# Kernel tuning notes

Measured on AMD Instinct MI355X. Metric: run time of the kernel, lower is better.

## Reference

```python
import jax, jax.numpy as jnp
import numpy as np

JITTER = 1e-6
ND = 20       # num_draws
STEPS = 10    # num_steps
G = 100       # num_gammas: PG truncation terms
NUM_CLASSES = 2


def _rbf(X, outputscale, lengthscale):
    x2 = jnp.sum(X * X, axis=-1)
    d2 = jnp.maximum(x2[:, None] + x2[None, :] - 2.0 * (X @ X.T), 0.0)
    return outputscale * jnp.exp(-0.5 * d2 / (lengthscale * lengthscale))


def _chol(K):
    return jnp.linalg.cholesky(K + JITTER * jnp.eye(K.shape[-1], dtype=K.dtype))


def _pg_draw(key, c):
    # PG(1, c) via truncated infinite gamma convolution (G terms):
    # omega = (1/(2 pi^2)) * sum_k Exp(1) / ((k-1/2)^2 + c^2/(4 pi^2))
    ks = jnp.arange(1, G + 1, dtype=c.dtype)
    denom = (ks - 0.5) ** 2 + (c[..., None] ** 2) / (4.0 * jnp.pi ** 2)
    e = jax.random.exponential(key, c.shape + (G,), dtype=c.dtype)
    return jnp.sum(e / denom, axis=-1) / (2.0 * jnp.pi ** 2)


def reference(X, Y, outputscale, lengthscale):
    N = X.shape[0]
    os_ = outputscale[0]
    ls = lengthscale[0]
    K = _rbf(X, os_, ls)                          # [N,N]
    Kinv = jnp.linalg.inv(K + JITTER * jnp.eye(N, dtype=X.dtype))
    L = _chol(K)
    mu = jnp.zeros((N,), X.dtype)                 # zero mean GP
    Kinv_mu = Kinv @ mu
    y_oh = 1.0 - jax.nn.one_hot(Y, NUM_CLASSES, dtype=X.dtype)
    kappa = y_oh[:, 0] - 0.5                      # binary => 1 stick, N_sb = 1

    key = jax.random.key(42)
    k_init, k_om0, k_loop = jax.random.split(key, 3)

    # initial Gibbs state: f ~ N(mu, K) per draw
    eps0 = jax.random.normal(k_init, (ND, N), X.dtype)
    f = mu[None, :] + jnp.einsum('ij,dj->di', L, eps0)
    omega = jax.lax.stop_gradient(_pg_draw(k_om0, jax.lax.stop_gradient(f)))

    def body(state, kk):
        omega_c, f_c = state
        k1, k2 = jax.random.split(kk)
        A = Kinv[None] + jax.vmap(jnp.diag)(omega_c)         # [ND,N,N]
        sigma = jnp.linalg.inv(A)
        mu_t = jnp.einsum('dij,j->di', sigma, kappa + Kinv_mu)
        Lt = _chol(sigma)
        eps = jax.random.normal(k1, (ND, N), X.dtype)
        f_new = mu_t + jnp.einsum('dij,dj->di', Lt, eps)
        omega_new = jax.lax.stop_gradient(_pg_draw(k2, jax.lax.stop_gradient(f_new)))
        return (omega_new, f_new), None

    (omega, f), _ = jax.lax.scan(body, (omega, f), jax.random.split(k_loop, STEPS))

    # marginal log likelihood given omega (PG draws are constants)
    om = jnp.clip(omega, 1e-16)                  # [ND,N]
    Sigma_z = K[None] + jax.vmap(jnp.diag)(1.0 / om)
    Lz = _chol(Sigma_z)
    z = kappa[None, :] / om
    diff = z - mu[None, :]
    sol = jax.scipy.linalg.solve_triangular(Lz, diff[..., None], lower=True)[..., 0]
    quad = jnp.sum(sol * sol, axis=-1)
    logdet = jnp.sum(jnp.log(jnp.diagonal(Lz, axis1=-2, axis2=-1)), axis=-1)
    log2pi = float(np.log(2.0 * np.pi))
    logp = -0.5 * quad - logdet - 0.5 * N * log2pi
    mll = (logp + 0.5 * N * log2pi
           - 0.5 * jnp.sum(jnp.log(om), axis=-1)
           + 0.5 * jnp.sum(kappa[None, :] ** 2 / om, axis=-1)
           - N * float(np.log(2.0)))
    nmll = -jnp.mean(mll)
    return nmll / N


def setup_inputs() -> dict:
    key = jax.random.key(0)
    kx, ky, ko, kl = jax.random.split(key, 4)
    X = jax.random.normal(kx, (1024, 64), jnp.float32)
    Y = jax.random.randint(ky, (1024,), 0, 2)
    outputscale = jax.random.uniform(ko, (1,), jnp.float32) + 0.5
    # rescale lengthscale to ~sqrt(d) so exp(-d2/2ls^2) doesn't underflow
    lengthscale = (jax.random.uniform(kl, (1,), jnp.float32) + 0.5) * 8.0
    return {"X": X, "Y": Y, "outputscale": outputscale, "lengthscale": lengthscale}
```

## Files before the change

### kernel.cpp

```cpp
#include <hip/hip_runtime.h>
#include <stdint.h>

#define NPTS 1024
#define NDRAWS 20
#define NSTEPS 10
#define NG 100
#define PARTITIONABLE 1

#define TRI(i) (((i) * ((i) + 1)) / 2)
#define NTRI 136
#define AST ((size_t)NTRI * 4096)

typedef unsigned int u32;

__host__ __device__ static inline void tf2x32(u32 k0, u32 k1, u32 x0, u32 x1, u32* o0, u32* o1){
  u32 ks2 = k0 ^ k1 ^ 0x1BD11BDAu;
  x0 += k0; x1 += k1;
#define TFR(r) { x0 += x1; x1 = (x1 << r) | (x1 >> (32 - r)); x1 ^= x0; }
  TFR(13) TFR(15) TFR(26) TFR(6)
  x0 += k1; x1 += ks2 + 1u;
  TFR(17) TFR(29) TFR(16) TFR(24)
  x0 += ks2; x1 += k0 + 2u;
  TFR(13) TFR(15) TFR(26) TFR(6)
  x0 += k0; x1 += k1 + 3u;
  TFR(17) TFR(29) TFR(16) TFR(24)
  x0 += k1; x1 += ks2 + 4u;
  TFR(13) TFR(15) TFR(26) TFR(6)
  x0 += ks2; x1 += k0 + 5u;
#undef TFR
  *o0 = x0; *o1 = x1;
}

__device__ static inline u32 rand32(u32 ka, u32 kb, u32 i, u32 total){
  u32 a, b;
#if PARTITIONABLE
  (void)total;
  tf2x32(ka, kb, 0u, i, &a, &b);
  return a ^ b;
#else
  u32 h = total >> 1;
  if (i < h){ tf2x32(ka, kb, i, i + h, &a, &b); return a; }
  else      { tf2x32(ka, kb, i - h, i, &a, &b); return b; }
#endif
}

__device__ static inline float u01f(u32 bits){
  return __uint_as_float(0x3F800000u | (bits >> 9)) - 1.0f;
}

__device__ static inline float erfinv32(float x){
  float w = -log1pf(-x * x);
  float p;
  if (w < 5.0f){
    w -= 2.5f;
// ... 291 lines not shown
#pragma unroll
      for (int b = 0; b < 4; ++b) ac2[a][b] += av[a] * bv[b];
  }
#pragma unroll
  for (int a = 0; a < 4; ++a)
#pragma unroll
    for (int b = 0; b < 4; ++b)
      Td[(size_t)(I * 64 + ty * 4 + a) * NPTS + J * 64 + tx * 4 + b] = -ac2[a][b];
}

__global__ __launch_bounds__(256) void k_syrk_kinv_flip(const double* Td, float* Kinvp){
  int a0, b0; tri_decode(blockIdx.x, a0, b0);
  int ti = b0, tj = a0;
  int kmin = tj;
  __shared__ double Ta[64][65];
  __shared__ double Tb[64][65];
  int tid = threadIdx.x, tx = tid & 15, ty = tid >> 4;
  double acc[4][4];
#pragma unroll
  for (int a = 0; a < 4; ++a)
#pragma unroll
    for (int b = 0; b < 4; ++b) acc[a][b] = 0.0;
  for (int K = kmin; K < 16; ++K){
    __syncthreads();
    for (int idx = tid; idx < 4096; idx += 256){
      int r = idx >> 6, c = idx & 63;
      Ta[r][c] = Td[(size_t)(K * 64 + r) * NPTS + ti * 64 + c];
      Tb[r][c] = Td[(size_t)(K * 64 + r) * NPTS + tj * 64 + c];
    }
    __syncthreads();
    for (int k = 0; k < 64; ++k){
      double av[4], bv[4];
#pragma unroll
      for (int a = 0; a < 4; ++a) av[a] = Ta[k][ty * 4 + a];
#pragma unroll
      for (int b = 0; b < 4; ++b) bv[b] = Tb[k][tx * 4 + b];
#pragma unroll
      for (int a = 0; a < 4; ++a)
#pragma unroll
        for (int b = 0; b < 4; ++b) acc[a][b] += av[a] * bv[b];
    }
  }
  int tileR = 15 - ti, tileC = 15 - tj;
  float* out = Kinvp + (size_t)(TRI(tileR) + tileC) * 4096;
#pragma unroll
  for (int a = 0; a < 4; ++a)
#pragma unroll
    for (int b = 0; b < 4; ++b){
      int rin = 63 - (ty * 4 + a), cin = 63 - (tx * 4 + b);
      out[rin * 64 + cin] = (float)acc[a][b];
    }
}

__global__ __launch_bounds__(256) void k_buildA(const float* Kinvp, const float* omega, float* Ab,
                                                int c0, int clip){
  int d = c0 + blockIdx.y;
  float* A = Ab + (size_t)blockIdx.y * AST;
  int idx4 = blockIdx.x * 256 + threadIdx.x;
  float4 v = ((const float4*)Kinvp)[idx4];
  int tile = idx4 >> 10;
  int ti, tj; tri_decode(tile, ti, tj);
  if (ti == tj){
    int e = (idx4 & 1023) * 4;
    int r = e >> 6, c = e & 63;
    if (c <= r && r < c + 4){
      float om = omega[(size_t)d * NPTS + (NPTS - 1 - (ti * 64 + r))];
      if (clip) om = fmaxf(om, 1e-16f);
      ((float*)&v)[r - c] += om;
    }
  }
  ((float4*)A)[idx4] = v;
}

__global__ __launch_bounds__(256) void k_diag0(float* Ab, float* Dinv){
  float* M = Ab + (size_t)blockIdx.x * AST;
  float* DI = Dinv + (size_t)blockIdx.x * 16 * 4096;
  __shared__ float t[64][65];
  __shared__ float Xs[64][65];
  __shared__ float diagL[64];
  int tid = threadIdx.x;
  for (int idx = tid; idx < 1024; idx += 256){
    float4 v = ((const float4*)M)[idx];
    int e = idx * 4, r = e >> 6, c = e & 63;
    t[r][c] = v.x; t[r][c + 1] = v.y; t[r][c + 2] = v.z; t[r][c + 3] = v.w;
  }
  __syncthreads();
  chol_inv_64t<float, 65>(&t[0][0], &Xs[0][0], &diagL[0], tid);
  for (int idx = tid; idx < 1024; idx += 256){
    int e = idx * 4, r = e >> 6, c = e & 63;
    float4 v, w;
    v.x = (c     <= r) ? t[r][c]     : 0.f;
    v.y = (c + 1 <= r) ? t[r][c + 1] : 0.f;
    v.z = (c + 2 <= r) ? t[r][c + 2] : 0.f;
    v.w = (c + 3 <= r) ? t[r][c + 3] : 0.f;
    w.x = Xs[r][c]; w.y = Xs[r][c + 1]; w.z = Xs[r][c + 2]; w.w = Xs[r][c + 3];
    ((float4*)M)[idx] = v;
    ((float4*)DI)[idx] = w;
  }
}

__global__ __launch_bounds__(256) void k_panel(float* Ab, const float* Dinv, int p){
  float* M = Ab + (size_t)blockIdx.y * AST;
  const float* DI = Dinv + ((size_t)blockIdx.y * 16 + p) * 4096;
  int rt = p + 1 + blockIdx.x;
  float* R = M + (size_t)(TRI(rt) + p) * 4096;
  __shared__ __align__(16) float Rst[64 * 68];
  __shared__ __align__(16) float Dst[64 * 68];
  int tid = threadIdx.x;
  for (int idx = tid; idx < 1024; idx += 256){
    float4 v = ((const float4*)R)[idx];
    float4 w = ((const float4*)DI)[idx];
    int e = idx * 4, r = e >> 6, c = e & 63;
    Rst[(c + 0) * 68 + r] = v.x; Rst[(c + 1) * 68 + r] = v.y;
    Rst[(c + 2) * 68 + r] = v.z; Rst[(c + 3) * 68 + r] = v.w;
    Dst[(c + 0) * 68 + r] = w.x; Dst[(c + 1) * 68 + r] = w.y;
    Dst[(c + 2) * 68 + r] = w.z; Dst[(c + 3) * 68 + r] = w.w;
  }
  __syncthreads();
  int tx = tid & 15, ty = tid >> 4;
  float acc[4][4];
#pragma unroll
  for (int a = 0; a < 4; ++a)
#pragma unroll
    for (int b = 0; b < 4; ++b) acc[a][b] = 0.f;
  for (int k = 0; k < 64; ++k){
    float4 av4 = *(const float4*)&Rst[k * 68 + ty * 4];
    float4 bv4 = *(const float4*)&Dst[k * 68 + tx * 4];
    float av[4] = {av4.x, av4.y, av4.z, av4.w};
    float bv[4] = {bv4.x, bv4.y, bv4.z, bv4.w};
#pragma unroll
    for (int a = 0; a < 4; ++a)
#pragma unroll
      for (int b = 0; b < 4; ++b) acc[a][b] += av[a] * bv[b];
  }
#pragma unroll
  for (int a = 0; a < 4; ++a){
    float4 v;
    v.x = acc[a][0]; v.y = acc[a][1]; v.z = acc[a][2]; v.w = acc[a][3];
    *((float4*)&R[(size_t)(ty * 4 + a) * 64 + tx * 4]) = v;
  }
}

__global__ __launch_bounds__(256) void k_update_diag(float* Ab, float* Dinv, int p){
  float* M = Ab + (size_t)blockIdx.y * AST;
  __shared__ __align__(16) float Pat[64 * 68];
  __shared__ __align__(16) float Pbt[64 * 68];
  __shared__ float diagL[64];
  int t0, t1; tri_decode(blockIdx.x, t0, t1);
  int bi = p + 1 + t0, bj = p + 1 + t1;
  const float* La = M + (size_t)(TRI(bi) + p) * 4096;
  const float* Lb = M + (size_t)(TRI(bj) + p) * 4096;
  float* Atile = M + (size_t)(TRI(bi) + bj) * 4096;
  int tid = threadIdx.x;
  for (int idx = tid; idx < 1024; idx += 256){
    float4 v = ((const float4*)La)[idx];
    float4 w = ((const float4*)Lb)[idx];
    int e = idx * 4, r = e >> 6, c = e & 63;
    Pat[(c + 0) * 68 + r] = v.x; Pat[(c + 1) * 68 + r] = v.y;
    Pat[(c + 2) * 68 + r] = v.z; Pat[(c + 3) * 68 + r] = v.w;
    Pbt[(c + 0) * 68 + r] = w.x; Pbt[(c + 1) * 68 + r] = w.y;
    Pbt[(c + 2) * 68 + r] = w.z; Pbt[(c + 3) * 68 + r] = w.w;
  }
  __syncthreads();
  int tx = tid & 15, ty = tid >> 4;
  float acc[4][4];
#pragma unroll
  for (int a = 0; a < 4; ++a)
#pragma unroll
    for (int b = 0; b < 4; ++b) acc[a][b] = 0.f;
  for (int k = 0; k < 64; ++k){
    float4 av4 = *(const float4*)&Pat[k * 68 + ty * 4];
    float4 bv4 = *(const float4*)&Pbt[k * 68 + tx * 4];
    float av[4] = {av4.x, av4.y, av4.z, av4.w};
    float bv[4] = {bv4.x, bv4.y, bv4.z, bv4.w};
#pragma unroll
    for (int a = 0; a < 4; ++a)
#pragma unroll
      for (int b = 0; b < 4; ++b) acc[a][b] += av[a] * bv[b];
  }
  if (blockIdx.x == 0){
    __syncthreads();
    for (int idx = tid; idx < 1024; idx += 256){
      float4 v = ((const float4*)Atile)[idx];
      int e = idx * 4, r = e >> 6, c = e & 63;
      Pat[r * 68 + c] = v.x; Pat[r * 68 + c + 1] = v.y;
      Pat[r * 68 + c + 2] = v.z; Pat[r * 68 + c + 3] = v.w;
    }
    __syncthreads();
#pragma unroll
    for (int a = 0; a < 4; ++a)
#pragma unroll
      for (int b = 0; b < 4; ++b)
        Pat[(ty * 4 + a) * 68 + tx * 4 + b] -= acc[a][b];
    __syncthreads();
    chol_inv_64t<float, 68>(Pat, Pbt, &diagL[0], tid);
    float* DI = Dinv + ((size_t)blockIdx.y * 16 + (p + 1)) * 4096;
    for (int idx = tid; idx < 1024; idx += 256){
      int e = idx * 4, r = e >> 6, c = e & 63;
      float4 v, w;
      v.x = (c     <= r) ? Pat[r * 68 + c]     : 0.f;
      v.y = (c + 1 <= r) ? Pat[r * 68 + c + 1] : 0.f;
      v.z = (c + 2 <= r) ? Pat[r * 68 + c + 2] : 0.f;
      v.w = (c + 3 <= r) ? Pat[r * 68 + c + 3] : 0.f;
      w.x = Pbt[r * 68 + c]; w.y = Pbt[r * 68 + c + 1];
      w.z = Pbt[r * 68 + c + 2]; w.w = Pbt[r * 68 + c + 3];
      ((float4*)Atile)[idx] = v;
      ((float4*)DI)[idx] = w;
    }
  } else {
#pragma unroll
    for (int a = 0; a < 4; ++a){
      float4 v = *((const float4*)&Atile[(size_t)(ty * 4 + a) * 64 + tx * 4]);
      v.x -= acc[a][0]; v.y -= acc[a][1]; v.z -= acc[a][2]; v.w -= acc[a][3];
      *((float4*)&Atile[(size_t)(ty * 4 + a) * 64 + tx * 4]) = v;
    }
  }
}

static void run_chol_f(float* A, float* Dinv, int batch, hipStream_t s){
  k_diag0<<<dim3(batch), 256, 0, s>>>(A, Dinv);
  for (int p = 0; p < 15; ++p){
    int nrb = 15 - p;
    k_panel<<<dim3(nrb, batch), 256, 0, s>>>(A, Dinv, p);
    k_update_diag<<<dim3(nrb * (nrb + 1) / 2, batch), 256, 0, s>>>(A, Dinv, p);
  }
}

__global__ __launch_bounds__(256) void k_step_solve(const float* Ab, const float* DinvF,
                                                    const float* kappaf, const float* eps,
                                                    float* fbuf, int c0){
  int d0 = blockIdx.x, d = c0 + d0;
  const float* L = Ab + (size_t)d0 * AST;
  const float* DI = DinvF + (size_t)d0 * 16 * 4096;
  __shared__ float z1[NPTS], z2[NPTS];
  __shared__ float buf[2][64 * 65];
  __shared__ float p1[4][64], p2[4][64];
  int tid = threadIdx.x;
  float4 rg[4];
  auto loadDI = [&](int p){
#pragma unroll
    for (int j = 0; j < 4; ++j)
      rg[j] = *(const float4*)&DI[p * 4096 + j * 1024 + tid * 4];
  };
  auto loadL = [&](int row, int col){
    const float* T = L + (size_t)(TRI(row) + col) * 4096;
#pragma unroll
    for (int j = 0; j < 4; ++j)
      rg[j] = *(const float4*)&T[j * 1024 + tid * 4];
  };
  auto store = [&](int cur){
#pragma unroll
    for (int j = 0; j < 4; ++j){
      int e = j * 1024 + tid * 4; int r = e >> 6, c = e & 63;
      float* b = &buf[cur][r * 65 + c];
      b[0] = rg[j].x; b[1] = rg[j].y; b[2] = rg[j].z; b[3] = rg[j].w;
    }
  };
  for (int i = tid; i < NPTS; i += 256){
    z1[i] = kappaf[i];
    z2[NPTS - 1 - i] = eps[(size_t)d * NPTS + i];
  }
  loadDI(0);
  int cur = 0;
  for (int p = 0; p < 16; ++p){
    for (int rb = p; rb < 16; ++rb){
      store(cur);
      int np = p, nrb = rb + 1;
      if (nrb >= 16){ np = p + 1; nrb = np; }
      if (np < 16){ if (nrb == np) loadDI(np); else loadL(nrb, np); }
      __syncthreads();
      int rr = tid & 63, q = tid >> 6;
      float s = 0.f;
#pragma unroll
      for (int cc = 0; cc < 16; ++cc)
        s += buf[cur][rr * 65 + q * 16 + cc] * z1[p * 64 + q * 16 + cc];
      p1[q][rr] = s;
      __syncthreads();
      if (tid < 64){
        float v = p1[0][tid] + p1[1][tid] + p1[2][tid] + p1[3][tid];
        if (rb == p) z1[p * 64 + tid] = v;
        else z1[rb * 64 + tid] -= v;
      }
      __syncthreads();
      cur ^= 1;
    }
  }
  loadDI(15);
  for (int p = 15; p >= 0; --p){
    for (int cb = p; cb >= 0; --cb){
      store(cur);
      int np = p, ncb = cb - 1;
      if (ncb < 0){ np = p - 1; ncb = np; }
      if (np >= 0){ if (ncb == np) loadDI(np); else loadL(np, ncb); }
      __syncthreads();
      int cc = tid & 63, q = tid >> 6;
      float s1 = 0.f, s2 = 0.f;
#pragma unroll
      for (int rr = 0; rr < 16; ++rr){
        float t = buf[cur][(q * 16 + rr) * 65 + cc];
        s1 += t * z1[p * 64 + q * 16 + rr];
        s2 += t * z2[p * 64 + q * 16 + rr];
      }
      p1[q][cc] = s1; p2[q][cc] = s2;
      __syncthreads();
      if (tid < 64){
        float v1 = p1[0][tid] + p1[1][tid] + p1[2][tid] + p1[3][tid];
        float v2 = p2[0][tid] + p2[1][tid] + p2[2][tid] + p2[3][tid];
        if (cb == p){ z1[p * 64 + tid] = v1; z2[p * 64 + tid] = v2; }
        else { z1[cb * 64 + tid] -= v1; z2[cb * 64 + tid] -= v2; }
      }
      __syncthreads();
      cur ^= 1;
    }
  }
  for (int i = tid; i < NPTS; i += 256)
    fbuf[(size_t)d * NPTS + i] = z1[NPTS - 1 - i] + z2[NPTS - 1 - i];
}

__global__ __launch_bounds__(256) void k_final3(const float* Ab, const float* DinvF,
                                                const float* kappaf, const float* ldetK,
                                                float* mll, int c0){
  int d0 = blockIdx.x, d = c0 + d0;
  const float* L = Ab + (size_t)d0 * AST;
  const float* DI = DinvF + (size_t)d0 * 16 * 4096;
  __shared__ float z[NPTS];
  __shared__ float buf[2][64 * 65];
  __shared__ float part[4][64];
  __shared__ float redq[4];
  int tid = threadIdx.x;
  float4 rg[4];
  auto loadDI = [&](int p){
#pragma unroll
    for (int j = 0; j < 4; ++j)
      rg[j] = *(const float4*)&DI[p * 4096 + j * 1024 + tid * 4];
  };
  auto loadL = [&](int rbrow, int pcol){
    const float* T = L + (size_t)(TRI(rbrow) + pcol) * 4096;
#pragma unroll
    for (int j = 0; j < 4; ++j)
      rg[j] = *(const float4*)&T[j * 1024 + tid * 4];
  };
  auto store = [&](int cur){
#pragma unroll
    for (int j = 0; j < 4; ++j){
      int e = j * 1024 + tid * 4; int r = e >> 6, c = e & 63;
      float* b = &buf[cur][r * 65 + c];
      b[0] = rg[j].x; b[1] = rg[j].y; b[2] = rg[j].z; b[3] = rg[j].w;
    }
  };
  for (int i = tid; i < NPTS; i += 256) z[i] = kappaf[i];
  loadDI(0);
  int cur = 0;
  float ldacc = 0.f;
  for (int p = 0; p < 16; ++p){
    for (int rb = p; rb < 16; ++rb){
      store(cur);
      int np = p, nrb = rb + 1;
      if (nrb >= 16){ np = p + 1; nrb = np; }
      if (np < 16){ if (nrb == np) loadDI(np); else loadL(nrb, np); }
      __syncthreads();
      if (rb == p && tid < 64) ldacc += logf(buf[cur][tid * 65 + tid]);
      int rr = tid & 63, q = tid >> 6;
      float s = 0.f;
#pragma unroll
      for (int cc = 0; cc < 16; ++cc)
        s += buf[cur][rr * 65 + q * 16 + cc] * z[p * 64 + q * 16 + cc];
      part[q][rr] = s;
      __syncthreads();
      if (tid < 64){
        float v = part[0][tid] + part[1][tid] + part[2][tid] + part[3][tid];
        if (rb == p) z[p * 64 + tid] = v;
        else z[rb * 64 + tid] -= v;
      }
      __syncthreads();
      cur ^= 1;
    }
  }
  float q2 = 0.f;
  for (int i = tid; i < NPTS; i += 256) q2 += z[i] * z[i];
  int wid = tid >> 6, lane = tid & 63;
  for (int o = 32; o; o >>= 1) q2 += __shfl_down(q2, o);
  if (lane == 0) redq[wid] = q2;
  __syncthreads();
  if (tid < 64){
    float ldv = ldacc;
    for (int o = 32; o; o >>= 1) ldv += __shfl_down(ldv, o);
    if (tid == 0){
      float q2t = redq[0] + redq[1] + redq[2] + redq[3];
      mll[d] = 0.5f * q2t + ldv - 0.5f * ldetK[0] - 709.7827128933839f;
    }
  }
}

__global__ __launch_bounds__(256) void k_gen_eps(u32 ka, u32 kb, float* eps){
  int i = blockIdx.x * 256 + threadIdx.x;
  if (i >= NDRAWS * NPTS) return;
  u32 bits = rand32(ka, kb, (u32)i, (u32)(NDRAWS * NPTS));
  eps[i] = normal_from_bits(bits);
}

__global__ __launch_bounds__(256) void k_init_f2(const float* Lf, const float* eps, float* f){
  int d = blockIdx.y, rb = blockIdx.x;
  __shared__ float tile[64][65];
  __shared__ float ev[64];
  __shared__ float part[4][64];
  int tid = threadIdx.x;
  int r = tid & 63, q = tid >> 6;
  float acc = 0.f;
  for (int kt = 0; kt <= rb; ++kt){
    __syncthreads();
#pragma unroll
    for (int j = 0; j < 4; ++j){
      int e = j * 1024 + tid * 4; int rr = e >> 6, cc = e & 63;
      float4 v = *(const float4*)&Lf[(size_t)(rb * 64 + rr) * NPTS + kt * 64 + cc];
      tile[rr][cc] = v.x; tile[rr][cc + 1] = v.y; tile[rr][cc + 2] = v.z; tile[rr][cc + 3] = v.w;
    }
    if (tid < 64) ev[tid] = eps[(size_t)d * NPTS + kt * 64 + tid];
    __syncthreads();
    int cmax = (kt == rb) ? (r + 1) : 64;
    for (int cc = q * 16; cc < q * 16 + 16; ++cc){
      if (cc < cmax) acc += tile[r][cc] * ev[cc];
    }
  }
  part[q][r] = acc;
  __syncthreads();
  if (tid < 64){
    float s = part[0][tid] + part[1][tid] + part[2][tid] + part[3][tid];
    f[(size_t)d * NPTS + rb * 64 + tid] = s;
  }
}

__global__ __launch_bounds__(256) void k_pg(u32 ka, u32 kb, const float* f, float* omega){
  int idx = blockIdx.x * 256 + threadIdx.x;
  if (idx >= NDRAWS * NPTS) return;
  float c = f[idx];
  float c2w = (c * c) / 39.47841760435743f;
  float sum = 0.f;
  u32 base = (u32)idx * NG;
  for (int g = 0; g < NG; ++g){
    u32 bits = rand32(ka, kb, base + (u32)g, (u32)(NDRAWS * NPTS * NG));
    float u = u01f(bits);
    float e = -log1pf(-u);
    float kk = (float)g + 0.5f;
// ... 25 lines not shown
}

extern "C" void kernel_launch(void* const* d_in, const int* in_sizes, int n_in,
                              void* d_out, int out_size, void* d_ws, size_t ws_size,
                              hipStream_t stream){
  const float* X  = (const float*)d_in[0];
  const int*   Y  = (const int*)d_in[1];
  const float* osp = (const float*)d_in[2];
  const float* lsp = (const float*)d_in[3];
  float* out = (float*)d_out;

  const size_t NN = (size_t)NPTS * NPTS;
  char* p = (char*)d_ws;
  float* Kinvp  = (float*)p;  p += AST * 4;
  float* omega  = (float*)p;  p += (size_t)NDRAWS * NPTS * 4;
  float* fbuf   = (float*)p;  p += (size_t)NDRAWS * NPTS * 4;
  float* epsb   = (float*)p;  p += (size_t)NDRAWS * NPTS * 4;
  float* kappaf = (float*)p;  p += NPTS * 4;
  float* x2     = (float*)p;  p += NPTS * 4;
  float* mll    = (float*)p;  p += 128;
  float* ldetK  = (float*)p;  p += 128;
  uintptr_t ip = (uintptr_t)p; ip = (ip + 255) & ~(uintptr_t)255;
  char* cb = (char*)ip;

  double* Ld    = (double*)cb;
  double* Td    = (double*)(cb + NN * 8);
  double* DinvD = (double*)(cb + NN * 16);
  float*  Lf    = (float*)(cb + NN * 16 + (size_t)16 * 4096 * 8);
  double* Gslc  = (double*)(cb + NN * 16 + (size_t)16 * 4096 * 8 + NN * 4);

  size_t rem = ws_size - (size_t)(cb - (char*)d_ws);
  const size_t PER_DRAW = AST * 4 + (size_t)16 * 4096 * 4;
  int CH = (int)(rem / PER_DRAW);
  if (CH > NDRAWS) CH = NDRAWS;
  if (CH < 1) CH = 1;
  float* bufA  = (float*)cb;
  float* dinvF = (float*)(cb + (size_t)CH * AST * 4);

  u32 r3A[3], r3B[3];
  host_split(0u, 42u, 3, r3A, r3B);
  u32 kiA = r3A[0], kiB = r3B[0];
  u32 koA = r3A[1], koB = r3B[1];
  u32 klA = r3A[2], klB = r3B[2];
  u32 kkA[NSTEPS], kkB[NSTEPS];
  host_split(klA, klB, NSTEPS, kkA, kkB);
  u32 k1A[NSTEPS], k1B[NSTEPS], k2A[NSTEPS], k2B[NSTEPS];
  for (int t = 0; t < NSTEPS; ++t){
    u32 sA[2], sB[2];
    host_split(kkA[t], kkB[t], 2, sA, sB);
    k1A[t] = sA[0]; k1B[t] = sB[0];
    k2A[t] = sA[1]; k2B[t] = sB[1];
  }

  k_prep<<<dim3(4), 256, 0, stream>>>(X, Y, x2, kappaf);
  k_computeK<<<dim3(64, 64), dim3(16, 16), 0, stream>>>(X, x2, osp, lsp, Ld);
  run_chol_d(Ld, DinvD, stream);
  k_castL<<<dim3(4096), 256, 0, stream>>>(Ld, Lf);
  k_logdetK<<<dim3(1), 256, 0, stream>>>(Ld, ldetK);
  k_trinv_copy_diag<<<dim3(16), 256, 0, stream>>>(DinvD, Td);
  for (int lev = 1; lev < 16; ++lev){
    k_trinv_part<<<dim3(16 - lev, lev), 256, 0, stream>>>(Ld, Td, Gslc, lev);
    k_trinv_fin<<<dim3(16 - lev), 256, 0, stream>>>(Td, Gslc, lev);
  }
  k_syrk_kinv_flip<<<dim3(NTRI), 256, 0, stream>>>(Td, Kinvp);

  k_gen_eps<<<dim3(80), 256, 0, stream>>>(kiA, kiB, epsb);
  k_init_f2<<<dim3(16, NDRAWS), 256, 0, stream>>>(Lf, epsb, fbuf);
  k_pg<<<dim3(80), 256, 0, stream>>>(koA, koB, fbuf, omega);

  for (int t = 0; t < NSTEPS; ++t){
    k_gen_eps<<<dim3(80), 256, 0, stream>>>(k1A[t], k1B[t], epsb);
    for (int c0 = 0; c0 < NDRAWS; c0 += CH){
      int nb = NDRAWS - c0 < CH ? NDRAWS - c0 : CH;
      k_buildA<<<dim3(544, nb), 256, 0, stream>>>(Kinvp, omega, bufA, c0, 0);
      run_chol_f(bufA, dinvF, nb, stream);
      k_step_solve<<<dim3(nb), 256, 0, stream>>>(bufA, dinvF, kappaf, epsb, fbuf, c0);
    }
    k_pg<<<dim3(80), 256, 0, stream>>>(k2A[t], k2B[t], fbuf, omega);
  }

  for (int c0 = 0; c0 < NDRAWS; c0 += CH){
    int nb = NDRAWS - c0 < CH ? NDRAWS - c0 : CH;
    k_buildA<<<dim3(544, nb), 256, 0, stream>>>(Kinvp, omega, bufA, c0, 1);
    run_chol_f(bufA, dinvF, nb, stream);
    k_final3<<<dim3(nb), 256, 0, stream>>>(bufA, dinvF, kappaf, ldetK, mll, c0);
  }
  k_out<<<dim3(1), 64, 0, stream>>>(mll, out);
}
```

Baseline: 23.16 ms.

## Fuse per-step Gibbs kernels into one persistent cooperative kernel with grid syncs

The eps generation, A assembly, blocked Cholesky (diag/panel/update phases), solve and PG draw for each chunk are merged into a single cooperative kernel. Grid-wide syncs separate the phases instead of dozens of separate kernel launches. This is meant to remove launch overhead and tail gaps across the roughly 30 launches per chunk per step. In exchange, grid size is capped at a few blocks per CU, and each grid.sync has its own cost. Phases with little work, like diag0 with nb blocks, leave most blocks idle.

```diff
diff --git a/kernel.cpp b/kernel.cpp
--- a/kernel.cpp
+++ b/kernel.cpp
@@ -1,5 +1,8 @@
 #include <hip/hip_runtime.h>
+#include <hip/hip_cooperative_groups.h>
 #include <stdint.h>
+
+namespace cg = cooperative_groups;
 
 #define NPTS 1024
 #define NDRAWS 20
@@ -397,343 +400,422 @@
     }
 }
 
-__global__ __launch_bounds__(256) void k_buildA(const float* Kinvp, const float* omega, float* Ab,
-                                                int c0, int clip){
-  int d = c0 + blockIdx.y;
-  float* A = Ab + (size_t)blockIdx.y * AST;
-  int idx4 = blockIdx.x * 256 + threadIdx.x;
-  float4 v = ((const float4*)Kinvp)[idx4];
-  int tile = idx4 >> 10;
-  int ti, tj; tri_decode(tile, ti, tj);
-  if (ti == tj){
-    int e = (idx4 & 1023) * 4;
-    int r = e >> 6, c = e & 63;
-    if (c <= r && r < c + 4){
-      float om = omega[(size_t)d * NPTS + (NPTS - 1 - (ti * 64 + r))];
-      if (clip) om = fmaxf(om, 1e-16f);
-      ((float*)&v)[r - c] += om;
-    }
-  }
-  ((float4*)A)[idx4] = v;
-}
-
-__global__ __launch_bounds__(256) void k_diag0(float* Ab, float* Dinv){
-  float* M = Ab + (size_t)blockIdx.x * AST;
-  float* DI = Dinv + (size_t)blockIdx.x * 16 * 4096;
-  __shared__ float t[64][65];
-  __shared__ float Xs[64][65];
-  __shared__ float diagL[64];
-  int tid = threadIdx.x;
-  for (int idx = tid; idx < 1024; idx += 256){
-    float4 v = ((const float4*)M)[idx];
-    int e = idx * 4, r = e >> 6, c = e & 63;
-    t[r][c] = v.x; t[r][c + 1] = v.y; t[r][c + 2] = v.z; t[r][c + 3] = v.w;
-  }
-  __syncthreads();
-  chol_inv_64t<float, 65>(&t[0][0], &Xs[0][0], &diagL[0], tid);
-  for (int idx = tid; idx < 1024; idx += 256){
-    int e = idx * 4, r = e >> 6, c = e & 63;
-    float4 v, w;
-    v.x = (c     <= r) ? t[r][c]     : 0.f;
-    v.y = (c + 1 <= r) ? t[r][c + 1] : 0.f;
-    v.z = (c + 2 <= r) ? t[r][c + 2] : 0.f;
-    v.w = (c + 3 <= r) ? t[r][c + 3] : 0.f;
-    w.x = Xs[r][c]; w.y = Xs[r][c + 1]; w.z = Xs[r][c + 2]; w.w = Xs[r][c + 3];
-    ((float4*)M)[idx] = v;
-    ((float4*)DI)[idx] = w;
-  }
-}
-
-__global__ __launch_bounds__(256) void k_panel(float* Ab, const float* Dinv, int p){
-  float* M = Ab + (size_t)blockIdx.y * AST;
-  const float* DI = Dinv + ((size_t)blockIdx.y * 16 + p) * 4096;
-  int rt = p + 1 + blockIdx.x;
-  float* R = M + (size_t)(TRI(rt) + p) * 4096;
-  __shared__ __align__(16) float Rst[64 * 68];
-  __shared__ __align__(16) float Dst[64 * 68];
-  int tid = threadIdx.x;
-  for (int idx = tid; idx < 1024; idx += 256){
-    float4 v = ((const float4*)R)[idx];
-    float4 w = ((const float4*)DI)[idx];
-    int e = idx * 4, r = e >> 6, c = e & 63;
-    Rst[(c + 0) * 68 + r] = v.x; Rst[(c + 1) * 68 + r] = v.y;
-    Rst[(c + 2) * 68 + r] = v.z; Rst[(c + 3) * 68 + r] = v.w;
-    Dst[(c + 0) * 68 + r] = w.x; Dst[(c + 1) * 68 + r] = w.y;
-    Dst[(c + 2) * 68 + r] = w.z; Dst[(c + 3) * 68 + r] = w.w;
-  }
-  __syncthreads();
-  int tx = tid & 15, ty = tid >> 4;
-  float acc[4][4];
-#pragma unroll
-  for (int a = 0; a < 4; ++a)
-#pragma unroll
-    for (int b = 0; b < 4; ++b) acc[a][b] = 0.f;
-  for (int k = 0; k < 64; ++k){
-    float4 av4 = *(const float4*)&Rst[k * 68 + ty * 4];
-    float4 bv4 = *(const float4*)&Dst[k * 68 + tx * 4];
-    float av[4] = {av4.x, av4.y, av4.z, av4.w};
-    float bv[4] = {bv4.x, bv4.y, bv4.z, bv4.w};
-#pragma unroll
-    for (int a = 0; a < 4; ++a)
-#pragma unroll
-      for (int b = 0; b < 4; ++b) acc[a][b] += av[a] * bv[b];
-  }
-#pragma unroll
-  for (int a = 0; a < 4; ++a){
-    float4 v;
-    v.x = acc[a][0]; v.y = acc[a][1]; v.z = acc[a][2]; v.w = acc[a][3];
-    *((float4*)&R[(size_t)(ty * 4 + a) * 64 + tx * 4]) = v;
-  }
-}
-
-__global__ __launch_bounds__(256) void k_update_diag(float* Ab, float* Dinv, int p){
-  float* M = Ab + (size_t)blockIdx.y * AST;
-  __shared__ __align__(16) float Pat[64 * 68];
-  __shared__ __align__(16) float Pbt[64 * 68];
-  __shared__ float diagL[64];
-  int t0, t1; tri_decode(blockIdx.x, t0, t1);
-  int bi = p + 1 + t0, bj = p + 1 + t1;
-  const float* La = M + (size_t)(TRI(bi) + p) * 4096;
-  const float* Lb = M + (size_t)(TRI(bj) + p) * 4096;
-  float* Atile = M + (size_t)(TRI(bi) + bj) * 4096;
-  int tid = threadIdx.x;
-  for (int idx = tid; idx < 1024; idx += 256){
-    float4 v = ((const float4*)La)[idx];
-    float4 w = ((const float4*)Lb)[idx];
-    int e = idx * 4, r = e >> 6, c = e & 63;
-    Pat[(c + 0) * 68 + r] = v.x; Pat[(c + 1) * 68 + r] = v.y;
-    Pat[(c + 2) * 68 + r] = v.z; Pat[(c + 3) * 68 + r] = v.w;
-    Pbt[(c + 0) * 68 + r] = w.x; Pbt[(c + 1) * 68 + r] = w.y;
-    Pbt[(c + 2) * 68 + r] = w.z; Pbt[(c + 3) * 68 + r] = w.w;
-  }
-  __syncthreads();
-  int tx = tid & 15, ty = tid >> 4;
-  float acc[4][4];
-#pragma unroll
-  for (int a = 0; a < 4; ++a)
-#pragma unroll
-    for (int b = 0; b < 4; ++b) acc[a][b] = 0.f;
-  for (int k = 0; k < 64; ++k){
-    float4 av4 = *(const float4*)&Pat[k * 68 + ty * 4];
-    float4 bv4 = *(const float4*)&Pbt[k * 68 + tx * 4];
-    float av[4] = {av4.x, av4.y, av4.z, av4.w};
-    float bv[4] = {bv4.x, bv4.y, bv4.z, bv4.w};
-#pragma unroll
-    for (int a = 0; a < 4; ++a)
-#pragma unroll
-      for (int b = 0; b < 4; ++b) acc[a][b] += av[a] * bv[b];
-  }
-  if (blockIdx.x == 0){
-    __syncthreads();
+
+__device__ inline void ph_geneps(u32 ka, u32 kb, float* eps, int c0, int nb, int tid){
+  int total = nb * NPTS;
+  for (int b0 = blockIdx.x * 256; b0 < total; b0 += gridDim.x * 256){
+    int i = b0 + tid;
+    if (i < total){
+      int g = c0 * NPTS + i;
+      u32 bits = rand32(ka, kb, (u32)g, (u32)(NDRAWS * NPTS));
+      eps[g] = normal_from_bits(bits);
+    }
+  }
+}
+
+__device__ inline void ph_pg(u32 ka, u32 kb, const float* f, float* omega, int c0, int nb, int tid){
+  int total = nb * NPTS;
+  for (int b0 = blockIdx.x * 256; b0 < total; b0 += gridDim.x * 256){
+    int i = b0 + tid;
+    if (i < total){
+      int gidx = c0 * NPTS + i;
+      float c = f[gidx];
+      float c2w = (c * c) / 39.47841760435743f;
+      float sum = 0.f;
+      u32 base = (u32)gidx * NG;
+      for (int g = 0; g < NG; ++g){
+        u32 bits = rand32(ka, kb, base + (u32)g, (u32)(NDRAWS * NPTS * NG));
+        float u = u01f(bits);
+        float e = -log1pf(-u);
+        float kk = (float)g + 0.5f;
+        sum += e / (kk * kk + c2w);
+      }
+      omega[gidx] = sum / 19.739208802178716f;
+    }
+  }
+}
+
+__device__ inline void ph_buildA(const float* Kinvp, const float* omega, float* Ab,
+                                 int c0, int nb, int clip, int tid){
+  for (int task = blockIdx.x; task < 544 * nb; task += gridDim.x){
+    int dd = task / 544, blk = task - dd * 544;
+    int d = c0 + dd;
+    float* A = Ab + (size_t)dd * AST;
+    int idx4 = blk * 256 + tid;
+    float4 v = ((const float4*)Kinvp)[idx4];
+    int tile = idx4 >> 10;
+    int ti, tj; tri_decode(tile, ti, tj);
+    if (ti == tj){
+      int e = (idx4 & 1023) * 4;
+      int r = e >> 6, c = e & 63;
+      if (c <= r && r < c + 4){
+        float om = omega[(size_t)d * NPTS + (NPTS - 1 - (ti * 64 + r))];
+        if (clip) om = fmaxf(om, 1e-16f);
+        ((float*)&v)[r - c] += om;
+      }
+    }
+    ((float4*)A)[idx4] = v;
+  }
+}
+
+__device__ inline void ph_diag0(float* Ab, float* Dinv, int nb, int tid,
+                                float* shT, float* shX, float* dgl){
+  for (int task = blockIdx.x; task < nb; task += gridDim.x){
+    float* M = Ab + (size_t)task * AST;
+    float* DI = Dinv + (size_t)task * 16 * 4096;
     for (int idx = tid; idx < 1024; idx += 256){
-      float4 v = ((const float4*)Atile)[idx];
+      float4 v = ((const float4*)M)[idx];
       int e = idx * 4, r = e >> 6, c = e & 63;
-      Pat[r * 68 + c] = v.x; Pat[r * 68 + c + 1] = v.y;
-      Pat[r * 68 + c + 2] = v.z; Pat[r * 68 + c + 3] = v.w;
-    }
-    __syncthreads();
-#pragma unroll
-    for (int a = 0; a < 4; ++a)
-#pragma unroll
-      for (int b = 0; b < 4; ++b)
-        Pat[(ty * 4 + a) * 68 + tx * 4 + b] -= acc[a][b];
-    __syncthreads();
-    chol_inv_64t<float, 68>(Pat, Pbt, &diagL[0], tid);
-    float* DI = Dinv + ((size_t)blockIdx.y * 16 + (p + 1)) * 4096;
+      shT[r * 68 + c] = v.x; shT[r * 68 + c + 1] = v.y;
+      shT[r * 68 + c + 2] = v.z; shT[r * 68 + c + 3] = v.w;
+    }
+    __syncthreads();
+    chol_inv_64t<float, 68>(shT, shX, dgl, tid);
     for (int idx = tid; idx < 1024; idx += 256){
       int e = idx * 4, r = e >> 6, c = e & 63;
       float4 v, w;
-      v.x = (c     <= r) ? Pat[r * 68 + c]     : 0.f;
-      v.y = (c + 1 <= r) ? Pat[r * 68 + c + 1] : 0.f;
-      v.z = (c + 2 <= r) ? Pat[r * 68 + c + 2] : 0.f;
-      v.w = (c + 3 <= r) ? Pat[r * 68 + c + 3] : 0.f;
-      w.x = Pbt[r * 68 + c]; w.y = Pbt[r * 68 + c + 1];
-      w.z = Pbt[r * 68 + c + 2]; w.w = Pbt[r * 68 + c + 3];
-      ((float4*)Atile)[idx] = v;
+      v.x = (c     <= r) ? shT[r * 68 + c]     : 0.f;
+      v.y = (c + 1 <= r) ? shT[r * 68 + c + 1] : 0.f;
+      v.z = (c + 2 <= r) ? shT[r * 68 + c + 2] : 0.f;
+      v.w = (c + 3 <= r) ? shT[r * 68 + c + 3] : 0.f;
+      w.x = shX[r * 68 + c]; w.y = shX[r * 68 + c + 1];
+      w.z = shX[r * 68 + c + 2]; w.w = shX[r * 68 + c + 3];
+      ((float4*)M)[idx] = v;
       ((float4*)DI)[idx] = w;
     }
+    __syncthreads();
+  }
+}
+
+__device__ inline void ph_panel(float* Ab, const float* Dinv, int p, int nb, int tid,
+                                float* Rst, float* Dst){
+  int nrb = 15 - p;
+  int tx = tid & 15, ty = tid >> 4;
+  for (int task = blockIdx.x; task < nrb * nb; task += gridDim.x){
+    int dd = task / nrb, rto = task - dd * nrb;
+    float* M = Ab + (size_t)dd * AST;
+    const float* DI = Dinv + ((size_t)dd * 16 + p) * 4096;
+    int rt = p + 1 + rto;
+    float* R = M + (size_t)(TRI(rt) + p) * 4096;
+    for (int idx = tid; idx < 1024; idx += 256){
+      float4 v = ((const float4*)R)[idx];
+      float4 w = ((const float4*)DI)[idx];
+      int e = idx * 4, r = e >> 6, c = e & 63;
+      Rst[(c + 0) * 68 + r] = v.x; Rst[(c + 1) * 68 + r] = v.y;
+      Rst[(c + 2) * 68 + r] = v.z; Rst[(c + 3) * 68 + r] = v.w;
+      Dst[(c + 0) * 68 + r] = w.x; Dst[(c + 1) * 68 + r] = w.y;
+      Dst[(c + 2) * 68 + r] = w.z; Dst[(c + 3) * 68 + r] = w.w;
+    }
+    __syncthreads();
+    float acc[4][4];
+#pragma unroll
+    for (int a = 0; a < 4; ++a)
+#pragma unroll
+      for (int b = 0; b < 4; ++b) acc[a][b] = 0.f;
+    for (int k = 0; k < 64; ++k){
+      float4 av4 = *(const float4*)&Rst[k * 68 + ty * 4];
+      float4 bv4 = *(const float4*)&Dst[k * 68 + tx * 4];
+      float av[4] = {av4.x, av4.y, av4.z, av4.w};
+      float bv[4] = {bv4.x, bv4.y, bv4.z, bv4.w};
+#pragma unroll
+      for (int a = 0; a < 4; ++a)
+#pragma unroll
+        for (int b = 0; b < 4; ++b) acc[a][b] += av[a] * bv[b];
+    }
+#pragma unroll
+    for (int a = 0; a < 4; ++a){
+      float4 v;
+      v.x = acc[a][0]; v.y = acc[a][1]; v.z = acc[a][2]; v.w = acc[a][3];
+      *((float4*)&R[(size_t)(ty * 4 + a) * 64 + tx * 4]) = v;
+    }
+    __syncthreads();
+  }
+}
+
+__device__ inline void ph_update(float* Ab, float* Dinv, int p, int nb, int tid,
+                                 float* Pat, float* Pbt, float* dgl){
+  int nrb = 15 - p;
+  int ntri = nrb * (nrb + 1) / 2;
+  int tx = tid & 15, ty = tid >> 4;
+  for (int task = blockIdx.x; task < ntri * nb; task += gridDim.x){
+    int dd = task / ntri, tri = task - dd * ntri;
+    float* M = Ab + (size_t)dd * AST;
+    int t0, t1; tri_decode(tri, t0, t1);
+    int bi = p + 1 + t0, bj = p + 1 + t1;
+    const float* La = M + (size_t)(TRI(bi) + p) * 4096;
+    const float* Lb = M + (size_t)(TRI(bj) + p) * 4096;
+    float* Atile = M + (size_t)(TRI(bi) + bj) * 4096;
+    for (int idx = tid; idx < 1024; idx += 256){
+      float4 v = ((const float4*)La)[idx];
+      float4 w = ((const float4*)Lb)[idx];
+      int e = idx * 4, r = e >> 6, c = e & 63;
+      Pat[(c + 0) * 68 + r] = v.x; Pat[(c + 1) * 68 + r] = v.y;
+      Pat[(c + 2) * 68 + r] = v.z; Pat[(c + 3) * 68 + r] = v.w;
+      Pbt[(c + 0) * 68 + r] = w.x; Pbt[(c + 1) * 68 + r] = w.y;
+      Pbt[(c + 2) * 68 + r] = w.z; Pbt[(c + 3) * 68 + r] = w.w;
+    }
+    __syncthreads();
+    float acc[4][4];
+#pragma unroll
+    for (int a = 0; a < 4; ++a)
+#pragma unroll
+      for (int b = 0; b < 4; ++b) acc[a][b] = 0.f;
+    for (int k = 0; k < 64; ++k){
+      float4 av4 = *(const float4*)&Pat[k * 68 + ty * 4];
+      float4 bv4 = *(const float4*)&Pbt[k * 68 + tx * 4];
+      float av[4] = {av4.x, av4.y, av4.z, av4.w};
+      float bv[4] = {bv4.x, bv4.y, bv4.z, bv4.w};
+#pragma unroll
+      for (int a = 0; a < 4; ++a)
+#pragma unroll
+        for (int b = 0; b < 4; ++b) acc[a][b] += av[a] * bv[b];
+    }
+    if (tri == 0){
+      __syncthreads();
+      for (int idx = tid; idx < 1024; idx += 256){
+        float4 v = ((const float4*)Atile)[idx];
+        int e = idx * 4, r = e >> 6, c = e & 63;
+        Pat[r * 68 + c] = v.x; Pat[r * 68 + c + 1] = v.y;
+        Pat[r * 68 + c + 2] = v.z; Pat[r * 68 + c + 3] = v.w;
+      }
+      __syncthreads();
+#pragma unroll
+      for (int a = 0; a < 4; ++a)
+#pragma unroll
+        for (int b = 0; b < 4; ++b)
+          Pat[(ty * 4 + a) * 68 + tx * 4 + b] -= acc[a][b];
+      __syncthreads();
+      chol_inv_64t<float, 68>(Pat, Pbt, dgl, tid);
+      float* DI = Dinv + ((size_t)dd * 16 + (p + 1)) * 4096;
+      for (int idx = tid; idx < 1024; idx += 256){
+        int e = idx * 4, r = e >> 6, c = e & 63;
+        float4 v, w;
+        v.x = (c     <= r) ? Pat[r * 68 + c]     : 0.f;
+        v.y = (c + 1 <= r) ? Pat[r * 68 + c + 1] : 0.f;
+        v.z = (c + 2 <= r) ? Pat[r * 68 + c + 2] : 0.f;
+        v.w = (c + 3 <= r) ? Pat[r * 68 + c + 3] : 0.f;
+        w.x = Pbt[r * 68 + c]; w.y = Pbt[r * 68 + c + 1];
+        w.z = Pbt[r * 68 + c + 2]; w.w = Pbt[r * 68 + c + 3];
+        ((float4*)Atile)[idx] = v;
+        ((float4*)DI)[idx] = w;
+      }
+      __syncthreads();
+    } else {
+#pragma unroll
+      for (int a = 0; a < 4; ++a){
+        float4 v = *((const float4*)&Atile[(size_t)(ty * 4 + a) * 64 + tx * 4]);
+        v.x -= acc[a][0]; v.y -= acc[a][1]; v.z -= acc[a][2]; v.w -= acc[a][3];
+        *((float4*)&Atile[(size_t)(ty * 4 + a) * 64 + tx * 4]) = v;
+      }
+      __syncthreads();
+    }
+  }
+}
+
+__device__ inline void ph_solve(const float* Ab, const float* DinvF, const float* kappaf,
+                                const float* eps, float* fbuf, int c0, int nb, int tid,
+                                float* smem){
+  float* z1  = smem;
+  float* z2  = smem + 1024;
+  float* bufp = smem + 2048;
+  float* pr1 = smem + 10368;
+  float* pr2 = smem + 10624;
+  for (int task = blockIdx.x; task < nb; task += gridDim.x){
+    int d0 = task, d = c0 + task;
+    const float* L = Ab + (size_t)d0 * AST;
+    const float* DI = DinvF + (size_t)d0 * 16 * 4096;
+    float4 rg[4];
+    auto loadDI = [&](int p){
+#pragma unroll
+      for (int j = 0; j < 4; ++j)
+        rg[j] = *(const float4*)&DI[p * 4096 + j * 1024 + tid * 4];
+    };
+    auto loadL = [&](int row, int col){
+      const float* T = L + (size_t)(TRI(row) + col) * 4096;
+#pragma unroll
+      for (int j = 0; j < 4; ++j)
+        rg[j] = *(const float4*)&T[j * 1024 + tid * 4];
+    };
+    auto store = [&](int cur){
+#pragma unroll
+      for (int j = 0; j < 4; ++j){
+        int e = j * 1024 + tid * 4; int r = e >> 6, c = e & 63;
+        float* b = &bufp[cur * 4160 + r * 65 + c];
+        b[0] = rg[j].x; b[1] = rg[j].y; b[2] = rg[j].z; b[3] = rg[j].w;
+      }
+    };
+    for (int i = tid; i < NPTS; i += 256){
+      z1[i] = kappaf[i];
+      z2[NPTS - 1 - i] = eps[(size_t)d * NPTS + i];
+    }
+    loadDI(0);
+    int cur = 0;
+    for (int p = 0; p < 16; ++p){
+      for (int rb = p; rb < 16; ++rb){
+        store(cur);
+        int np = p, nr2 = rb + 1;
+        if (nr2 >= 16){ np = p + 1; nr2 = np; }
+        if (np < 16){ if (nr2 == np) loadDI(np); else loadL(nr2, np); }
+        __syncthreads();
+        int rr = tid & 63, q = tid >> 6;
+        float s = 0.f;
+#pragma unroll
+        for (int cc = 0; cc < 16; ++cc)
+          s += bufp[cur * 4160 + rr * 65 + q * 16 + cc] * z1[p * 64 + q * 16 + cc];
+        pr1[q * 64 + rr] = s;
+        __syncthreads();
+        if (tid < 64){
+          float v = pr1[tid] + pr1[64 + tid] + pr1[128 + tid] + pr1[192 + tid];
+          if (rb == p) z1[p * 64 + tid] = v;
+          else z1[rb * 64 + tid] -= v;
+        }
+        __syncthreads();
+        cur ^= 1;
+      }
+    }
+    loadDI(15);
+    for (int p = 15; p >= 0; --p){
+      for (int cb = p; cb >= 0; --cb){
+        store(cur);
+        int np = p, ncb = cb - 1;
+        if (ncb < 0){ np = p - 1; ncb = np; }
+        if (np >= 0){ if (ncb == np) loadDI(np); else loadL(np, ncb); }
+        __syncthreads();
+        int cc2 = tid & 63, q = tid >> 6;
+        float s1 = 0.f, s2 = 0.f;
+#pragma unroll
+        for (int rr = 0; rr < 16; ++rr){
+          float t = bufp[cur * 4160 + (q * 16 + rr) * 65 + cc2];
+          s1 += t * z1[p * 64 + q * 16 + rr];
+          s2 += t * z2[p * 64 + q * 16 + rr];
+        }
+        pr1[q * 64 + cc2] = s1; pr2[q * 64 + cc2] = s2;
+        __syncthreads();
+        if (tid < 64){
+          float v1 = pr1[tid] + pr1[64 + tid] + pr1[128 + tid] + pr1[192 + tid];
+          float v2 = pr2[tid] + pr2[64 + tid] + pr2[128 + tid] + pr2[192 + tid];
+          if (cb == p){ z1[p * 64 + tid] = v1; z2[p * 64 + tid] = v2; }
+          else { z1[cb * 64 + tid] -= v1; z2[cb * 64 + tid] -= v2; }
+        }
+        __syncthreads();
+        cur ^= 1;
+      }
+    }
+    for (int i = tid; i < NPTS; i += 256)
+      fbuf[(size_t)d * NPTS + i] = z1[NPTS - 1 - i] + z2[NPTS - 1 - i];
+    __syncthreads();
+  }
+}
+
+__device__ inline void ph_final(const float* Ab, const float* DinvF, const float* kappaf,
+                                const float* ldetK, float* mll, int c0, int nb, int tid,
+                                float* smem){
+  float* z    = smem;
+  float* bufp = smem + 2048;
+  float* part = smem + 10368;
+  float* redq = smem + 10624;
+  for (int task = blockIdx.x; task < nb; task += gridDim.x){
+    int d0 = task, d = c0 + task;
+    const float* L = Ab + (size_t)d0 * AST;
+    const float* DI = DinvF + (size_t)d0 * 16 * 4096;
+    float4 rg[4];
+    auto loadDI = [&](int p){
+#pragma unroll
+      for (int j = 0; j < 4; ++j)
+        rg[j] = *(const float4*)&DI[p * 4096 + j * 1024 + tid * 4];
+    };
+    auto loadL = [&](int row, int col){
+      const float* T = L + (size_t)(TRI(row) + col) * 4096;
+#pragma unroll
+      for (int j = 0; j < 4; ++j)
+        rg[j] = *(const float4*)&T[j * 1024 + tid * 4];
+    };
+    auto store = [&](int cur){
+#pragma unroll
+      for (int j = 0; j < 4; ++j){
+        int e = j * 1024 + tid * 4; int r = e >> 6, c = e & 63;
+        float* b = &bufp[cur * 4160 + r * 65 + c];
+        b[0] = rg[j].x; b[1] = rg[j].y; b[2] = rg[j].z; b[3] = rg[j].w;
+      }
+    };
+    for (int i = tid; i < NPTS; i += 256) z[i] = kappaf[i];
+    loadDI(0);
+    int cur = 0;
+    float ldacc = 0.f;
+    for (int p = 0; p < 16; ++p){
+      for (int rb = p; rb < 16; ++rb){
+        store(cur);
+        int np = p, nr2 = rb + 1;
+        if (nr2 >= 16){ np = p + 1; nr2 = np; }
+        if (np < 16){ if (nr2 == np) loadDI(np); else loadL(nr2, np); }
+        __syncthreads();
+        if (rb == p && tid < 64) ldacc += logf(bufp[cur * 4160 + tid * 65 + tid]);
+        int rr = tid & 63, q = tid >> 6;
+        float s = 0.f;
+#pragma unroll
+        for (int cc = 0; cc < 16; ++cc)
+          s += bufp[cur * 4160 + rr * 65 + q * 16 + cc] * z[p * 64 + q * 16 + cc];
+        part[q * 64 + rr] = s;
+        __syncthreads();
+        if (tid < 64){
+          float v = part[tid] + part[64 + tid] + part[128 + tid] + part[192 + tid];
+          if (rb == p) z[p * 64 + tid] = v;
+          else z[rb * 64 + tid] -= v;
+        }
+        __syncthreads();
+        cur ^= 1;
+      }
+    }
+    float q2 = 0.f;
+    for (int i = tid; i < NPTS; i += 256) q2 += z[i] * z[i];
+    int wid = tid >> 6, lane = tid & 63;
+    for (int o = 32; o; o >>= 1) q2 += __shfl_down(q2, o);
+    if (lane == 0) redq[wid] = q2;
+    __syncthreads();
+    if (tid < 64){
+      float ldv = ldacc;
+      for (int o = 32; o; o >>= 1) ldv += __shfl_down(ldv, o);
+      if (tid == 0){
+        float q2t = redq[0] + redq[1] + redq[2] + redq[3];
+        mll[d] = 0.5f * q2t + ldv - 0.5f * ldetK[0] - 709.7827128933839f;
+      }
+    }
+    __syncthreads();
+  }
+}
+
+__global__ void __launch_bounds__(256) k_gibbs_coop(
+    float* bufA, float* dinvF, const float* Kinvp, float* omega,
+    const float* kappaf, float* epsb, float* fbuf,
+    const float* ldetK, float* mll, int c0, int nb, int mode,
+    u32 k1a, u32 k1b, u32 k2a, u32 k2b)
+{
+  cg::grid_group grid = cg::this_grid();
+  __shared__ __align__(16) float smem[10880];
+  int tid = threadIdx.x;
+  float* shA = smem;
+  float* shB = smem + 4352;
+  float* dgl = smem + 8704;
+  if (mode == 0){
+    ph_geneps(k1a, k1b, epsb, c0, nb, tid);
+    grid.sync();
+  }
+  ph_buildA(Kinvp, omega, bufA, c0, nb, mode, tid);
+  grid.sync();
+  ph_diag0(bufA, dinvF, nb, tid, shA, shB, dgl);
+  grid.sync();
+  for (int p = 0; p < 15; ++p){
+    ph_panel(bufA, dinvF, p, nb, tid, shA, shB);
+    grid.sync();
+    ph_update(bufA, dinvF, p, nb, tid, shA, shB, dgl);
+    grid.sync();
+  }
+  if (mode == 0){
+    ph_solve(bufA, dinvF, kappaf, epsb, fbuf, c0, nb, tid, smem);
+    grid.sync();
+    ph_pg(k2a, k2b, fbuf, omega, c0, nb, tid);
   } else {
-#pragma unroll
-    for (int a = 0; a < 4; ++a){
-      float4 v = *((const float4*)&Atile[(size_t)(ty * 4 + a) * 64 + tx * 4]);
-      v.x -= acc[a][0]; v.y -= acc[a][1]; v.z -= acc[a][2]; v.w -= acc[a][3];
-      *((float4*)&Atile[(size_t)(ty * 4 + a) * 64 + tx * 4]) = v;
-    }
-  }
-}
-
-static void run_chol_f(float* A, float* Dinv, int batch, hipStream_t s){
-  k_diag0<<<dim3(batch), 256, 0, s>>>(A, Dinv);
-  for (int p = 0; p < 15; ++p){
-    int nrb = 15 - p;
-    k_panel<<<dim3(nrb, batch), 256, 0, s>>>(A, Dinv, p);
-    k_update_diag<<<dim3(nrb * (nrb + 1) / 2, batch), 256, 0, s>>>(A, Dinv, p);
-  }
-}
-
-__global__ __launch_bounds__(256) void k_step_solve(const float* Ab, const float* DinvF,
-                                                    const float* kappaf, const float* eps,
-                                                    float* fbuf, int c0){
-  int d0 = blockIdx.x, d = c0 + d0;
-  const float* L = Ab + (size_t)d0 * AST;
-  const float* DI = DinvF + (size_t)d0 * 16 * 4096;
-  __shared__ float z1[NPTS], z2[NPTS];
-  __shared__ float buf[2][64 * 65];
-  __shared__ float p1[4][64], p2[4][64];
-  int tid = threadIdx.x;
-  float4 rg[4];
-  auto loadDI = [&](int p){
-#pragma unroll
-    for (int j = 0; j < 4; ++j)
-      rg[j] = *(const float4*)&DI[p * 4096 + j * 1024 + tid * 4];
-  };
-  auto loadL = [&](int row, int col){
-    const float* T = L + (size_t)(TRI(row) + col) * 4096;
-#pragma unroll
-    for (int j = 0; j < 4; ++j)
-      rg[j] = *(const float4*)&T[j * 1024 + tid * 4];
-  };
-  auto store = [&](int cur){
-#pragma unroll
-    for (int j = 0; j < 4; ++j){
-      int e = j * 1024 + tid * 4; int r = e >> 6, c = e & 63;
-      float* b = &buf[cur][r * 65 + c];
-      b[0] = rg[j].x; b[1] = rg[j].y; b[2] = rg[j].z; b[3] = rg[j].w;
-    }
-  };
-  for (int i = tid; i < NPTS; i += 256){
-    z1[i] = kappaf[i];
-    z2[NPTS - 1 - i] = eps[(size_t)d * NPTS + i];
-  }
-  loadDI(0);
-  int cur = 0;
-  for (int p = 0; p < 16; ++p){
-    for (int rb = p; rb < 16; ++rb){
-      store(cur);
-      int np = p, nrb = rb + 1;
-      if (nrb >= 16){ np = p + 1; nrb = np; }
-      if (np < 16){ if (nrb == np) loadDI(np); else loadL(nrb, np); }
-      __syncthreads();
-      int rr = tid & 63, q = tid >> 6;
-      float s = 0.f;
-#pragma unroll
-      for (int cc = 0; cc < 16; ++cc)
-        s += buf[cur][rr * 65 + q * 16 + cc] * z1[p * 64 + q * 16 + cc];
-      p1[q][rr] = s;
-      __syncthreads();
-      if (tid < 64){
-        float v = p1[0][tid] + p1[1][tid] + p1[2][tid] + p1[3][tid];
-        if (rb == p) z1[p * 64 + tid] = v;
-        else z1[rb * 64 + tid] -= v;
-      }
-      __syncthreads();
-      cur ^= 1;
-    }
-  }
-  loadDI(15);
-  for (int p = 15; p >= 0; --p){
-    for (int cb = p; cb >= 0; --cb){
-      store(cur);
-      int np = p, ncb = cb - 1;
-      if (ncb < 0){ np = p - 1; ncb = np; }
-      if (np >= 0){ if (ncb == np) loadDI(np); else loadL(np, ncb); }
-      __syncthreads();
-      int cc = tid & 63, q = tid >> 6;
-      float s1 = 0.f, s2 = 0.f;
-#pragma unroll
-      for (int rr = 0; rr < 16; ++rr){
-        float t = buf[cur][(q * 16 + rr) * 65 + cc];
-        s1 += t * z1[p * 64 + q * 16 + rr];
-        s2 += t * z2[p * 64 + q * 16 + rr];
-      }
-      p1[q][cc] = s1; p2[q][cc] = s2;
-      __syncthreads();
-      if (tid < 64){
-        float v1 = p1[0][tid] + p1[1][tid] + p1[2][tid] + p1[3][tid];
-        float v2 = p2[0][tid] + p2[1][tid] + p2[2][tid] + p2[3][tid];
-        if (cb == p){ z1[p * 64 + tid] = v1; z2[p * 64 + tid] = v2; }
-        else { z1[cb * 64 + tid] -= v1; z2[cb * 64 + tid] -= v2; }
-      }
-      __syncthreads();
-      cur ^= 1;
-    }
-  }
-  for (int i = tid; i < NPTS; i += 256)
-    fbuf[(size_t)d * NPTS + i] = z1[NPTS - 1 - i] + z2[NPTS - 1 - i];
-}
-
-__global__ __launch_bounds__(256) void k_final3(const float* Ab, const float* DinvF,
-                                                const float* kappaf, const float* ldetK,
-                                                float* mll, int c0){
-  int d0 = blockIdx.x, d = c0 + d0;
-  const float* L = Ab + (size_t)d0 * AST;
-  const float* DI = DinvF + (size_t)d0 * 16 * 4096;
-  __shared__ float z[NPTS];
-  __shared__ float buf[2][64 * 65];
-  __shared__ float part[4][64];
-  __shared__ float redq[4];
-  int tid = threadIdx.x;
-  float4 rg[4];
-  auto loadDI = [&](int p){
-#pragma unroll
-    for (int j = 0; j < 4; ++j)
-      rg[j] = *(const float4*)&DI[p * 4096 + j * 1024 + tid * 4];
-  };
-  auto loadL = [&](int rbrow, int pcol){
-    const float* T = L + (size_t)(TRI(rbrow) + pcol) * 4096;
-#pragma unroll
-    for (int j = 0; j < 4; ++j)
-      rg[j] = *(const float4*)&T[j * 1024 + tid * 4];
-  };
-  auto store = [&](int cur){
-#pragma unroll
-    for (int j = 0; j < 4; ++j){
-      int e = j * 1024 + tid * 4; int r = e >> 6, c = e & 63;
-      float* b = &buf[cur][r * 65 + c];
-      b[0] = rg[j].x; b[1] = rg[j].y; b[2] = rg[j].z; b[3] = rg[j].w;
-    }
-  };
-  for (int i = tid; i < NPTS; i += 256) z[i] = kappaf[i];
-  loadDI(0);
-  int cur = 0;
-  float ldacc = 0.f;
-  for (int p = 0; p < 16; ++p){
-    for (int rb = p; rb < 16; ++rb){
-      store(cur);
-      int np = p, nrb = rb + 1;
-      if (nrb >= 16){ np = p + 1; nrb = np; }
-      if (np < 16){ if (nrb == np) loadDI(np); else loadL(nrb, np); }
-      __syncthreads();
-      if (rb == p && tid < 64) ldacc += logf(buf[cur][tid * 65 + tid]);
-      int rr = tid & 63, q = tid >> 6;
-      float s = 0.f;
-#pragma unroll
-      for (int cc = 0; cc < 16; ++cc)
-        s += buf[cur][rr * 65 + q * 16 + cc] * z[p * 64 + q * 16 + cc];
-      part[q][rr] = s;
-      __syncthreads();
-      if (tid < 64){
-        float v = part[0][tid] + part[1][tid] + part[2][tid] + part[3][tid];
-        if (rb == p) z[p * 64 + tid] = v;
-        else z[rb * 64 + tid] -= v;
-      }
-      __syncthreads();
-      cur ^= 1;
-    }
-  }
-  float q2 = 0.f;
-  for (int i = tid; i < NPTS; i += 256) q2 += z[i] * z[i];
-  int wid = tid >> 6, lane = tid & 63;
-  for (int o = 32; o; o >>= 1) q2 += __shfl_down(q2, o);
-  if (lane == 0) redq[wid] = q2;
-  __syncthreads();
-  if (tid < 64){
-    float ldv = ldacc;
-    for (int o = 32; o; o >>= 1) ldv += __shfl_down(ldv, o);
-    if (tid == 0){
-      float q2t = redq[0] + redq[1] + redq[2] + redq[3];
-      mll[d] = 0.5f * q2t + ldv - 0.5f * ldetK[0] - 709.7827128933839f;
-    }
+    ph_final(bufA, dinvF, kappaf, ldetK, mll, c0, nb, tid, smem);
   }
 }
 
@@ -865,6 +947,12 @@
     k2A[t] = sA[1]; k2B[t] = sB[1];
   }
 
+  int maxb = 0;
+  if (hipOccupancyMaxActiveBlocksPerMultiprocessor(&maxb, k_gibbs_coop, 256, 0) != hipSuccess || maxb < 1)
+    maxb = 2;
+  if (maxb > 3) maxb = 3;
+  int G = maxb * 256;
+
   k_prep<<<dim3(4), 256, 0, stream>>>(X, Y, x2, kappaf);
   k_computeK<<<dim3(64, 64), dim3(16, 16), 0, stream>>>(X, x2, osp, lsp, Ld);
   run_chol_d(Ld, DinvD, stream);
@@ -881,22 +969,26 @@
   k_init_f2<<<dim3(16, NDRAWS), 256, 0, stream>>>(Lf, epsb, fbuf);
   k_pg<<<dim3(80), 256, 0, stream>>>(koA, koB, fbuf, omega);
 
+  int c0v, nbv, modev;
+  u32 a1, b1, a2, b2;
+  void* cargs[16] = {&bufA, &dinvF, &Kinvp, &omega, &kappaf, &epsb, &fbuf,
+                     &ldetK, &mll, &c0v, &nbv, &modev, &a1, &b1, &a2, &b2};
   for (int t = 0; t < NSTEPS; ++t){
-    k_gen_eps<<<dim3(80), 256, 0, stream>>>(k1A[t], k1B[t], epsb);
     for (int c0 = 0; c0 < NDRAWS; c0 += CH){
-      int nb = NDRAWS - c0 < CH ? NDRAWS - c0 : CH;
-      k_buildA<<<dim3(544, nb), 256, 0, stream>>>(Kinvp, omega, bufA, c0, 0);
-      run_chol_f(bufA, dinvF, nb, stream);
-      k_step_solve<<<dim3(nb), 256, 0, stream>>>(bufA, dinvF, kappaf, epsb, fbuf, c0);
-    }
-    k_pg<<<dim3(80), 256, 0, stream>>>(k2A[t], k2B[t], fbuf, omega);
+      c0v = c0;
+      nbv = (NDRAWS - c0 < CH) ? (NDRAWS - c0) : CH;
+      modev = 0;
+      a1 = k1A[t]; b1 = k1B[t]; a2 = k2A[t]; b2 = k2B[t];
+      hipLaunchCooperativeKernel((const void*)k_gibbs_coop, dim3(G), dim3(256), cargs, 0, stream);
+    }
   }
 
   for (int c0 = 0; c0 < NDRAWS; c0 += CH){
-    int nb = NDRAWS - c0 < CH ? NDRAWS - c0 : CH;
-    k_buildA<<<dim3(544, nb), 256, 0, stream>>>(Kinvp, omega, bufA, c0, 1);
-    run_chol_f(bufA, dinvF, nb, stream);
-    k_final3<<<dim3(nb), 256, 0, stream>>>(bufA, dinvF, kappaf, ldetK, mll, c0);
+    c0v = c0;
+    nbv = (NDRAWS - c0 < CH) ? (NDRAWS - c0) : CH;
+    modev = 1;
+    a1 = 0; b1 = 0; a2 = 0; b2 = 0;
+    hipLaunchCooperativeKernel((const void*)k_gibbs_coop, dim3(G), dim3(256), cargs, 0, stream);
   }
   k_out<<<dim3(1), 64, 0, stream>>>(mll, out);
 }
```

Result: slower. 41.40 ms (+78.8%).
